# Kernel optimization log

Hardware: AMD Instinct MI355X
Metric: run time of the kernel (lower is better)

The kernel has to match this reference:

```python
import jax, jax.numpy as jnp
import numpy as np

E, T, H, I, K = 32, 2048, 1024, 512, 4


def setup_inputs() -> dict:
    key = jax.random.key(0)
    k1, k2, k3, k4, k5 = jax.random.split(key, 5)
    hidden_states = jax.random.normal(k1, (T, H), dtype=jnp.float32)
    top_k_index = jax.random.randint(k2, (T, K), 0, E)
    w = jax.random.uniform(k3, (T, K), dtype=jnp.float32)
    top_k_weights = w / jnp.sum(w, axis=-1, keepdims=True)  # router-like normalized weights
    gate_up_proj = jax.random.normal(k4, (E, 2 * I, H), dtype=jnp.float32) * 0.02
    down_proj = jax.random.normal(k5, (E, H, I), dtype=jnp.float32) * 0.02
    return {
        "hidden_states": hidden_states,
        "top_k_index": top_k_index,
        "top_k_weights": top_k_weights,
        "gate_up_proj": gate_up_proj,
        "down_proj": down_proj,
    }


def reference(hidden_states, top_k_index, top_k_weights, gate_up_proj, down_proj):
    # Faithful to the eager MoE dispatch loop: for each expert e, gather the
    # tokens routed to it, run gate/up/down SwiGLU, scale by routing weight,
    # and scatter-add into the output. Expressed as a scan over experts with a
    # per-token routing weight that is 0 for unrouted tokens (identical math:
    # index_add over (token, slot) pairs == sum_k where(idx==e, w, 0)).
    num_experts = gate_up_proj.shape[0]
    inter = down_proj.shape[2]

    def expert_step(acc, xs):
        gup_w, down_w, e = xs  # [2I, H], [H, I], scalar expert id
        # combined routing weight per token for this expert: [T]
        w_tok = jnp.sum(jnp.where(top_k_index == e, top_k_weights, 0.0), axis=1)
        gu = hidden_states @ gup_w.T              # [T, 2I]
        gate, up = gu[:, :inter], gu[:, inter:]
        h = jax.nn.silu(gate) * up                # [T, I]
        out = h @ down_w.T                        # [T, H]
        return acc + out * w_tok[:, None], None

    init = jnp.zeros_like(hidden_states)
    final_hidden_states, _ = jax.lax.scan(
        expert_step, init,
        (gate_up_proj, down_proj, jnp.arange(num_experts)),
    )
    return final_hidden_states
```

## Files before the change

### kernel.cpp

```cpp
#include <hip/hip_runtime.h>

#define NE 32
#define NT 2048
#define NH 1024
#define NI 512
#define NK 4
#define CAP 512

typedef __attribute__((ext_vector_type(8))) short short8;
typedef __attribute__((ext_vector_type(4))) float floatx4;

static __device__ __forceinline__ unsigned pk_bf16(float x, float y) {
#if __has_builtin(__builtin_amdgcn_cvt_pk_bf16_f32)
    typedef __attribute__((ext_vector_type(2))) __bf16 bf16x2;
    union { bf16x2 v; unsigned u; } c;
    c.v = __builtin_amdgcn_cvt_pk_bf16_f32(x, y);
    return c.u;
#else
    union { float f; unsigned u; } a, b;
    a.f = x; b.f = y;
    unsigned ua = (a.u + 0x7fffu + ((a.u >> 16) & 1u)) >> 16;
    unsigned ub = (b.u + 0x7fffu + ((b.u >> 16) & 1u)) >> 16;
    return (ua & 0xffffu) | (ub << 16);
#endif
}

static __device__ __forceinline__ short8 pack8(const float* p) {
    union { unsigned u[4]; short8 s; } c;
    c.u[0] = pk_bf16(p[0], p[1]);
    c.u[1] = pk_bf16(p[2], p[3]);
    c.u[2] = pk_bf16(p[4], p[5]);
    c.u[3] = pk_bf16(p[6], p[7]);
    return c.s;
}

static __device__ __forceinline__ unsigned short bf16_1(float x) {
    return (unsigned short)(pk_bf16(x, 0.f) & 0xffffu);
}

__global__ void route_kernel(const int* __restrict__ idx,
                             const float* __restrict__ w,
                             int* __restrict__ counts,
                             int* __restrict__ tok,
                             float* __restrict__ wgt) {
    int tid = blockIdx.x * blockDim.x + threadIdx.x;
    if (tid >= NT * NK) return;
    int e = idx[tid];
    int pos = atomicAdd(&counts[e], 1);
    if (pos < CAP) {
        tok[e * CAP + pos] = tid;
        wgt[e * CAP + pos] = w[tid];
    }
}

__global__ void cvt_hidden(const float* __restrict__ hidden,
                           unsigned short* __restrict__ hb16) {
    size_t i = (size_t)(blockIdx.x * 256 + threadIdx.x) * 8;
    float tmp[8];
    *(floatx4*)tmp       = *(const floatx4*)(hidden + i);
    *(floatx4*)(tmp + 4) = *(const floatx4*)(hidden + i + 4);
    *(short8*)(hb16 + i) = pack8(tmp);
}

__global__ __launch_bounds__(256) void gateup_mfma(
    const unsigned short* __restrict__ hb16,
    const float* __restrict__ gup,
    const int* __restrict__ counts,
    const int* __restrict__ tok,
    unsigned short* __restrict__ hbuf)
{
    int e = blockIdx.z;
    int cnt = counts[e];
    int m0 = blockIdx.y * 128;
    if (m0 >= cnt) return;
    int j0 = blockIdx.x * 64;

    __shared__ __align__(16) char smem[36864];
    __shared__ int tks[128];

    short (*As)[72] = (short(*)[72])smem;
    short (*Bs)[72] = (short(*)[72])(smem + 18432);
    float (*upb)[64][68] = (float(*)[64][68])smem;

    int tid = threadIdx.x;
    if (tid < 128) {
        int mi = m0 + tid;
        tks[tid] = tok[e * CAP + (mi < cnt ? mi : m0)];
    }
    __syncthreads();

    int srow = tid >> 1;
    int shalf = tid & 1;
    const unsigned short* ag = hb16 + (size_t)(tks[srow] >> 2) * NH + shalf * 32;
    const float* gup_e = gup + (size_t)e * (2 * NI) * NH;
    int gj = (srow < 64) ? (j0 + srow) : (NI + j0 + (srow - 64));
    const float* bg = gup_e + (size_t)gj * NH + shalf * 32;

    int wave = tid >> 6, lane = tid & 63;
    int wm = wave >> 1;
    int wv = wave & 1;
    int lcol = lane & 15;
    int quad = lane >> 4;
    int lk = quad * 8;

    floatx4 acc[4][4];
#pragma unroll
    for (int a = 0; a < 4; a++)
#pragma unroll
        for (int b = 0; b < 4; b++) acc[a][b] = (floatx4){0.f, 0.f, 0.f, 0.f};

    for (int h0 = 0; h0 < NH; h0 += 64) {
#pragma unroll
        for (int q = 0; q < 4; q++)
            *(short8*)&As[srow][shalf * 32 + q * 8] =
                *(const short8*)(ag + h0 + q * 8);
#pragma unroll
        for (int q = 0; q < 4; q++) {
            float tmp[8];
            *(floatx4*)tmp       = *(const floatx4*)(bg + h0 + q * 8);
            *(floatx4*)(tmp + 4) = *(const floatx4*)(bg + h0 + q * 8 + 4);
            *(short8*)&Bs[srow][shalf * 32 + q * 8] = pack8(tmp);
        }
        __syncthreads();
#pragma unroll
        for (int ks = 0; ks < 2; ks++) {
            short8 af[4], bfr[4];
#pragma unroll
            for (int mt = 0; mt < 4; mt++)
                af[mt] = *(const short8*)&As[wm * 64 + mt * 16 + lcol][ks * 32 + lk];
#pragma unroll
            for (int nt = 0; nt < 4; nt++)
                bfr[nt] = *(const short8*)&Bs[wv * 64 + nt * 16 + lcol][ks * 32 + lk];
#pragma unroll
            for (int mt = 0; mt < 4; mt++)
#pragma unroll
                for (int nt = 0; nt < 4; nt++)
                    acc[mt][nt] = __builtin_amdgcn_mfma_f32_16x16x32_bf16(
                        af[mt], bfr[nt], acc[mt][nt], 0, 0, 0);
        }
        __syncthreads();
    }

    if (wv == 1) {
#pragma unroll
        for (int mt = 0; mt < 4; mt++)
#pragma unroll
            for (int nt = 0; nt < 4; nt++)
#pragma unroll
                for (int i = 0; i < 4; i++)
                    upb[wm][mt * 16 + quad * 4 + i][nt * 16 + lcol] = acc[mt][nt][i];
    }
    __syncthreads();
    if (wv == 0) {
#pragma unroll
        for (int mt = 0; mt < 4; mt++) {
#pragma unroll
            for (int i = 0; i < 4; i++) {
                int lm = mt * 16 + quad * 4 + i;
                int m = wm * 64 + lm;
                if (m0 + m < cnt) {
                    unsigned short* hp = hbuf + (size_t)tks[m] * NI + j0;
#pragma unroll
                    for (int nt = 0; nt < 4; nt++) {
                        float g = acc[mt][nt][i];
                        float u = upb[wm][lm][nt * 16 + lcol];
                        float h = g / (1.f + __expf(-g)) * u;
                        hp[nt * 16 + lcol] = bf16_1(h);
                    }
                }
            }
        }
    }
}

__global__ __launch_bounds__(256) void down_mfma(
    const unsigned short* __restrict__ hbuf,
    const float* __restrict__ down,
    const int* __restrict__ counts,
    const int* __restrict__ tok,
    const float* __restrict__ wgt,
    float* __restrict__ out)
{
    int e = blockIdx.z;
    int cnt = counts[e];
    int m0 = blockIdx.y * 128;
    if (m0 >= cnt) return;
    int n0 = blockIdx.x * 128;

    __shared__ __align__(16) short As[128][72];
    __shared__ __align__(16) short Bs[128][72];
    __shared__ int tks[128];
    __shared__ float wls[128];

    int tid = threadIdx.x;
    if (tid < 128) {
        int mi = m0 + tid;
        int src = e * CAP + (mi < cnt ? mi : m0);
        tks[tid] = tok[src];
        wls[tid] = wgt[src];
    }
    __syncthreads();

    int srow = tid >> 1;
    int shalf = tid & 1;
    const unsigned short* ag = hbuf + (size_t)tks[srow] * NI + shalf * 32;
    const float* down_e = down + (size_t)e * NH * NI;
    const float* bg = down_e + (size_t)(n0 + srow) * NI + shalf * 32;

    int wave = tid >> 6, lane = tid & 63;
    int wm = wave >> 1, wn = wave & 1;
    int lcol = lane & 15;
    int quad = lane >> 4;
    int lk = quad * 8;

    floatx4 acc[4][4];
#pragma unroll
    for (int a = 0; a < 4; a++)
#pragma unroll
        for (int b = 0; b < 4; b++) acc[a][b] = (floatx4){0.f, 0.f, 0.f, 0.f};

    for (int i0 = 0; i0 < NI; i0 += 64) {
#pragma unroll
        for (int q = 0; q < 4; q++)
            *(short8*)&As[srow][shalf * 32 + q * 8] =
                *(const short8*)(ag + i0 + q * 8);
#pragma unroll
        for (int q = 0; q < 4; q++) {
            float tmp[8];
            *(floatx4*)tmp       = *(const floatx4*)(bg + i0 + q * 8);
            *(floatx4*)(tmp + 4) = *(const floatx4*)(bg + i0 + q * 8 + 4);
            *(short8*)&Bs[srow][shalf * 32 + q * 8] = pack8(tmp);
        }
        __syncthreads();
#pragma unroll
        for (int ks = 0; ks < 2; ks++) {
            short8 af[4], bfr[4];
#pragma unroll
            for (int mt = 0; mt < 4; mt++)
                af[mt] = *(const short8*)&As[wm * 64 + mt * 16 + lcol][ks * 32 + lk];
#pragma unroll
            for (int nt = 0; nt < 4; nt++)
                bfr[nt] = *(const short8*)&Bs[wn * 64 + nt * 16 + lcol][ks * 32 + lk];
#pragma unroll
            for (int mt = 0; mt < 4; mt++)
#pragma unroll
                for (int nt = 0; nt < 4; nt++)
                    acc[mt][nt] = __builtin_amdgcn_mfma_f32_16x16x32_bf16(
                        af[mt], bfr[nt], acc[mt][nt], 0, 0, 0);
        }
        __syncthreads();
    }

#pragma unroll
    for (int mt = 0; mt < 4; mt++)
#pragma unroll
        for (int i = 0; i < 4; i++) {
            int m = wm * 64 + mt * 16 + quad * 4 + i;
            if (m0 + m < cnt) {
                int t = tks[m] >> 2;
                float wl = wls[m];
                float* op = out + (size_t)t * NH + n0 + wn * 64;
#pragma unroll
                for (int nt = 0; nt < 4; nt++)
                    atomicAdd(op + nt * 16 + lcol, acc[mt][nt][i] * wl);
            }
        }
}

extern "C" void kernel_launch(void* const* d_in, const int* in_sizes, int n_in,
                              void* d_out, int out_size, void* d_ws, size_t ws_size,
                              hipStream_t stream) {
    const float* hidden = (const float*)d_in[0];
    const int*   tk_idx = (const int*)d_in[1];
    const float* tk_w   = (const float*)d_in[2];
    const float* gup    = (const float*)d_in[3];
    const float* down   = (const float*)d_in[4];
    float* out = (float*)d_out;

    char* ws = (char*)d_ws;
    int*            counts = (int*)ws;
    int*            tok    = (int*)(ws + 256);
    float*          wgt    = (float*)(ws + 256 + NE * CAP * 4);
    unsigned short* hb16   = (unsigned short*)(ws + 256 + 2 * NE * CAP * 4);
    unsigned short* hbuf   = (unsigned short*)(ws + 256 + 2 * NE * CAP * 4
                                               + (size_t)NT * NH * 2);

    hipMemsetAsync(counts, 0, 256, stream);
    hipMemsetAsync(out, 0, (size_t)NT * NH * sizeof(float), stream);

    route_kernel<<<(NT * NK + 255) / 256, 256, 0, stream>>>(tk_idx, tk_w, counts, tok, wgt);
    cvt_hidden<<<(NT * NH / 8) / 256, 256, 0, stream>>>(hidden, hb16);

    dim3 gridG(NI / 64, CAP / 128, NE);
    gateup_mfma<<<gridG, 256, 0, stream>>>(hb16, gup, counts, tok, hbuf);

    dim3 gridD(NH / 128, CAP / 128, NE);
    down_mfma<<<gridD, 256, 0, stream>>>(hbuf, down, counts, tok, wgt, out);
}
```

Before: 402.6 us.

## Register-prefetch next K tile and coalesce global loads in both expert GEMMs

Both grouped GEMM kernels now issue the global loads for the next K tile into registers right after the barrier, so they overlap with the MFMA work on the current tile, then write them to shared memory at the start of the next iteration. The thread-to-element mapping is also changed so adjacent threads read adjacent 16-byte chunks of a row, giving coalesced accesses instead of each thread streaming half a row. The cost is more live registers for the prefetch buffers, which may reduce occupancy.

```diff
diff --git a/kernel.cpp b/kernel.cpp
--- a/kernel.cpp
+++ b/kernel.cpp
@@ -89,12 +89,18 @@
     }
     __syncthreads();
 
-    int srow = tid >> 1;
-    int shalf = tid & 1;
-    const unsigned short* ag = hb16 + (size_t)(tks[srow] >> 2) * NH + shalf * 32;
+    int arow_base = tid >> 3;
+    int acol = (tid & 7) * 8;
+    const unsigned short* ap[4];
+#pragma unroll
+    for (int p = 0; p < 4; p++)
+        ap[p] = hb16 + (size_t)(tks[p * 32 + arow_base] >> 2) * NH + acol;
+
+    int brow_base = tid >> 4;
+    int bcol = (tid & 15) * 4;
     const float* gup_e = gup + (size_t)e * (2 * NI) * NH;
-    int gj = (srow < 64) ? (j0 + srow) : (NI + j0 + (srow - 64));
-    const float* bg = gup_e + (size_t)gj * NH + shalf * 32;
+    const float* bp0 = gup_e + (size_t)(j0 + brow_base) * NH + bcol;
+#define GUP_OFF(p) ((size_t)(p) * 16 * NH + ((p) >= 4 ? (size_t)(NI - 64) * NH : (size_t)0))
 
     int wave = tid >> 6, lane = tid & 63;
     int wm = wave >> 1;
@@ -109,19 +115,32 @@
 #pragma unroll
         for (int b = 0; b < 4; b++) acc[a][b] = (floatx4){0.f, 0.f, 0.f, 0.f};
 
+    short8 ra[4];
+    float4 rb[8];
+#pragma unroll
+    for (int p = 0; p < 4; p++) ra[p] = *(const short8*)(ap[p]);
+#pragma unroll
+    for (int p = 0; p < 8; p++) rb[p] = *(const float4*)(bp0 + GUP_OFF(p));
+
     for (int h0 = 0; h0 < NH; h0 += 64) {
 #pragma unroll
-        for (int q = 0; q < 4; q++)
-            *(short8*)&As[srow][shalf * 32 + q * 8] =
-                *(const short8*)(ag + h0 + q * 8);
-#pragma unroll
-        for (int q = 0; q < 4; q++) {
-            float tmp[8];
-            *(floatx4*)tmp       = *(const floatx4*)(bg + h0 + q * 8);
-            *(floatx4*)(tmp + 4) = *(const floatx4*)(bg + h0 + q * 8 + 4);
-            *(short8*)&Bs[srow][shalf * 32 + q * 8] = pack8(tmp);
+        for (int p = 0; p < 4; p++)
+            *(short8*)&As[p * 32 + arow_base][acol] = ra[p];
+#pragma unroll
+        for (int p = 0; p < 8; p++) {
+            uint2 u;
+            u.x = pk_bf16(rb[p].x, rb[p].y);
+            u.y = pk_bf16(rb[p].z, rb[p].w);
+            *(uint2*)&Bs[p * 16 + brow_base][bcol] = u;
         }
         __syncthreads();
+        int hn = h0 + 64;
+        if (hn < NH) {
+#pragma unroll
+            for (int p = 0; p < 4; p++) ra[p] = *(const short8*)(ap[p] + hn);
+#pragma unroll
+            for (int p = 0; p < 8; p++) rb[p] = *(const float4*)(bp0 + GUP_OFF(p) + hn);
+        }
 #pragma unroll
         for (int ks = 0; ks < 2; ks++) {
             short8 af[4], bfr[4];
@@ -201,11 +220,18 @@
     }
     __syncthreads();
 
-    int srow = tid >> 1;
-    int shalf = tid & 1;
-    const unsigned short* ag = hbuf + (size_t)tks[srow] * NI + shalf * 32;
+    int arow_base = tid >> 3;
+    int acol = (tid & 7) * 8;
+    const unsigned short* ap[4];
+#pragma unroll
+    for (int p = 0; p < 4; p++)
+        ap[p] = hbuf + (size_t)tks[p * 32 + arow_base] * NI + acol;
+
+    int brow_base = tid >> 4;
+    int bcol = (tid & 15) * 4;
     const float* down_e = down + (size_t)e * NH * NI;
-    const float* bg = down_e + (size_t)(n0 + srow) * NI + shalf * 32;
+    const float* bp0 = down_e + (size_t)(n0 + brow_base) * NI + bcol;
+#define DN_OFF(p) ((size_t)(p) * 16 * NI)
 
     int wave = tid >> 6, lane = tid & 63;
     int wm = wave >> 1, wn = wave & 1;
@@ -219,19 +245,32 @@
 #pragma unroll
         for (int b = 0; b < 4; b++) acc[a][b] = (floatx4){0.f, 0.f, 0.f, 0.f};
 
+    short8 ra[4];
+    float4 rb[8];
+#pragma unroll
+    for (int p = 0; p < 4; p++) ra[p] = *(const short8*)(ap[p]);
+#pragma unroll
+    for (int p = 0; p < 8; p++) rb[p] = *(const float4*)(bp0 + DN_OFF(p));
+
     for (int i0 = 0; i0 < NI; i0 += 64) {
 #pragma unroll
-        for (int q = 0; q < 4; q++)
-            *(short8*)&As[srow][shalf * 32 + q * 8] =
-                *(const short8*)(ag + i0 + q * 8);
-#pragma unroll
-        for (int q = 0; q < 4; q++) {
-            float tmp[8];
-            *(floatx4*)tmp       = *(const floatx4*)(bg + i0 + q * 8);
-            *(floatx4*)(tmp + 4) = *(const floatx4*)(bg + i0 + q * 8 + 4);
-            *(short8*)&Bs[srow][shalf * 32 + q * 8] = pack8(tmp);
+        for (int p = 0; p < 4; p++)
+            *(short8*)&As[p * 32 + arow_base][acol] = ra[p];
+#pragma unroll
+        for (int p = 0; p < 8; p++) {
+            uint2 u;
+            u.x = pk_bf16(rb[p].x, rb[p].y);
+            u.y = pk_bf16(rb[p].z, rb[p].w);
+            *(uint2*)&Bs[p * 16 + brow_base][bcol] = u;
         }
         __syncthreads();
+        int in = i0 + 64;
+        if (in < NI) {
+#pragma unroll
+            for (int p = 0; p < 4; p++) ra[p] = *(const short8*)(ap[p] + in);
+#pragma unroll
+            for (int p = 0; p < 8; p++) rb[p] = *(const float4*)(bp0 + DN_OFF(p) + in);
+        }
 #pragma unroll
         for (int ks = 0; ks < 2; ks++) {
             short8 af[4], bfr[4];
```

After: 339.6 us. -15.6%, faster.

## Double-buffer LDS with register prefetch and XOR swizzle in both MoE GEMMs

Applied to the files above, without the earlier changes.

Both expert GEMM kernels now use double-buffered LDS tiles. The next K-slice is prefetched into registers while MFMAs run on the current buffer, so each iteration needs one barrier instead of two. The padded LDS rows are replaced by an XOR-swizzled layout to avoid bank conflicts, and gate-up now assigns gate and up columns to the same wave so SwiGLU runs in registers without an LDS exchange. Occupancy hints (launch_bounds 256,2) and clamping of count to capacity are added, at the cost of more registers and more LDS per block.

```diff
diff --git a/kernel.cpp b/kernel.cpp
--- a/kernel.cpp
+++ b/kernel.cpp
@@ -62,7 +62,8 @@
     *(short8*)(hb16 + i) = pack8(tmp);
 }
 
-__global__ __launch_bounds__(256) void gateup_mfma(
+
+__global__ __launch_bounds__(256, 2) void gateup_mfma(
     const unsigned short* __restrict__ hb16,
     const float* __restrict__ gup,
     const int* __restrict__ counts,
@@ -70,38 +71,40 @@
     unsigned short* __restrict__ hbuf)
 {
     int e = blockIdx.z;
-    int cnt = counts[e];
+    int cnt = counts[e]; if (cnt > CAP) cnt = CAP;
     int m0 = blockIdx.y * 128;
     if (m0 >= cnt) return;
     int j0 = blockIdx.x * 64;
 
-    __shared__ __align__(16) char smem[36864];
-    __shared__ int tks[128];
-
-    short (*As)[72] = (short(*)[72])smem;
-    short (*Bs)[72] = (short(*)[72])(smem + 18432);
-    float (*upb)[64][68] = (float(*)[64][68])smem;
+    __shared__ __align__(16) short As[2][128][64];
+    __shared__ __align__(16) short Bs[2][128][64];
 
     int tid = threadIdx.x;
-    if (tid < 128) {
-        int mi = m0 + tid;
-        tks[tid] = tok[e * CAP + (mi < cnt ? mi : m0)];
-    }
-    __syncthreads();
-
-    int srow = tid >> 1;
-    int shalf = tid & 1;
-    const unsigned short* ag = hb16 + (size_t)(tks[srow] >> 2) * NH + shalf * 32;
+    int sr = tid >> 3;
+    int sg = tid & 7;
+
+    const unsigned short* aptr[4];
+    short* awr[4];
+    const float* bptr[4];
+    short* bwr[4];
     const float* gup_e = gup + (size_t)e * (2 * NI) * NH;
-    int gj = (srow < 64) ? (j0 + srow) : (NI + j0 + (srow - 64));
-    const float* bg = gup_e + (size_t)gj * NH + shalf * 32;
+#pragma unroll
+    for (int p = 0; p < 4; p++) {
+        int r = p * 32 + sr;
+        int mi = m0 + r;
+        int tk = tok[e * CAP + (mi < cnt ? mi : m0)];
+        aptr[p] = hb16 + (size_t)(tk >> 2) * NH + sg * 8;
+        awr[p]  = &As[0][r][(sg ^ (r & 7)) * 8];
+        int gj = (r < 64) ? (j0 + r) : (NI + j0 + (r - 64));
+        bptr[p] = gup_e + (size_t)gj * NH + sg * 8;
+        bwr[p]  = &Bs[0][r][(sg ^ (r & 7)) * 8];
+    }
 
     int wave = tid >> 6, lane = tid & 63;
     int wm = wave >> 1;
-    int wv = wave & 1;
+    int wj = wave & 1;
     int lcol = lane & 15;
     int quad = lane >> 4;
-    int lk = quad * 8;
 
     floatx4 acc[4][4];
 #pragma unroll
@@ -109,28 +112,51 @@
 #pragma unroll
         for (int b = 0; b < 4; b++) acc[a][b] = (floatx4){0.f, 0.f, 0.f, 0.f};
 
-    for (int h0 = 0; h0 < NH; h0 += 64) {
-#pragma unroll
-        for (int q = 0; q < 4; q++)
-            *(short8*)&As[srow][shalf * 32 + q * 8] =
-                *(const short8*)(ag + h0 + q * 8);
-#pragma unroll
-        for (int q = 0; q < 4; q++) {
-            float tmp[8];
-            *(floatx4*)tmp       = *(const floatx4*)(bg + h0 + q * 8);
-            *(floatx4*)(tmp + 4) = *(const floatx4*)(bg + h0 + q * 8 + 4);
-            *(short8*)&Bs[srow][shalf * 32 + q * 8] = pack8(tmp);
-        }
-        __syncthreads();
+    short8 ra[4];
+    float4 rb[8];
+#pragma unroll
+    for (int p = 0; p < 4; p++) {
+        ra[p] = *(const short8*)(aptr[p]);
+        rb[2 * p]     = *(const float4*)(bptr[p]);
+        rb[2 * p + 1] = *(const float4*)(bptr[p] + 4);
+    }
+#pragma unroll
+    for (int p = 0; p < 4; p++) {
+        *(short8*)(awr[p]) = ra[p];
+        union { unsigned u[4]; short8 s; } c;
+        c.u[0] = pk_bf16(rb[2 * p].x, rb[2 * p].y);
+        c.u[1] = pk_bf16(rb[2 * p].z, rb[2 * p].w);
+        c.u[2] = pk_bf16(rb[2 * p + 1].x, rb[2 * p + 1].y);
+        c.u[3] = pk_bf16(rb[2 * p + 1].z, rb[2 * p + 1].w);
+        *(short8*)(bwr[p]) = c.s;
+    }
+#pragma unroll
+    for (int p = 0; p < 4; p++) {
+        ra[p] = *(const short8*)(aptr[p] + 64);
+        rb[2 * p]     = *(const float4*)(bptr[p] + 64);
+        rb[2 * p + 1] = *(const float4*)(bptr[p] + 68);
+    }
+    __syncthreads();
+
+    const int NIT = NH / 64;
+    for (int it = 0; it < NIT; ++it) {
+        int cur = it & 1;
+        int co = cur * 8192;
 #pragma unroll
         for (int ks = 0; ks < 2; ks++) {
             short8 af[4], bfr[4];
-#pragma unroll
-            for (int mt = 0; mt < 4; mt++)
-                af[mt] = *(const short8*)&As[wm * 64 + mt * 16 + lcol][ks * 32 + lk];
-#pragma unroll
-            for (int nt = 0; nt < 4; nt++)
-                bfr[nt] = *(const short8*)&Bs[wv * 64 + nt * 16 + lcol][ks * 32 + lk];
+            int q = ks * 4 + quad;
+#pragma unroll
+            for (int mt = 0; mt < 4; mt++) {
+                int R = wm * 64 + mt * 16 + lcol;
+                af[mt] = *(const short8*)&As[cur][R][(q ^ (R & 7)) * 8];
+            }
+#pragma unroll
+            for (int nt = 0; nt < 4; nt++) {
+                int R = (nt < 2) ? (wj * 32 + nt * 16 + lcol)
+                                 : (64 + wj * 32 + (nt - 2) * 16 + lcol);
+                bfr[nt] = *(const short8*)&Bs[cur][R][(q ^ (R & 7)) * 8];
+            }
 #pragma unroll
             for (int mt = 0; mt < 4; mt++)
 #pragma unroll
@@ -138,42 +164,52 @@
                     acc[mt][nt] = __builtin_amdgcn_mfma_f32_16x16x32_bf16(
                         af[mt], bfr[nt], acc[mt][nt], 0, 0, 0);
         }
-        __syncthreads();
-    }
-
-    if (wv == 1) {
-#pragma unroll
-        for (int mt = 0; mt < 4; mt++)
-#pragma unroll
-            for (int nt = 0; nt < 4; nt++)
-#pragma unroll
-                for (int i = 0; i < 4; i++)
-                    upb[wm][mt * 16 + quad * 4 + i][nt * 16 + lcol] = acc[mt][nt][i];
-    }
-    __syncthreads();
-    if (wv == 0) {
-#pragma unroll
-        for (int mt = 0; mt < 4; mt++) {
-#pragma unroll
-            for (int i = 0; i < 4; i++) {
-                int lm = mt * 16 + quad * 4 + i;
-                int m = wm * 64 + lm;
-                if (m0 + m < cnt) {
-                    unsigned short* hp = hbuf + (size_t)tks[m] * NI + j0;
-#pragma unroll
-                    for (int nt = 0; nt < 4; nt++) {
-                        float g = acc[mt][nt][i];
-                        float u = upb[wm][lm][nt * 16 + lcol];
-                        float h = g / (1.f + __expf(-g)) * u;
-                        hp[nt * 16 + lcol] = bf16_1(h);
-                    }
+        if (it + 1 < NIT) {
+            int no = (co ^ 8192);
+#pragma unroll
+            for (int p = 0; p < 4; p++) {
+                *(short8*)(awr[p] + no) = ra[p];
+                union { unsigned u[4]; short8 s; } c;
+                c.u[0] = pk_bf16(rb[2 * p].x, rb[2 * p].y);
+                c.u[1] = pk_bf16(rb[2 * p].z, rb[2 * p].w);
+                c.u[2] = pk_bf16(rb[2 * p + 1].x, rb[2 * p + 1].y);
+                c.u[3] = pk_bf16(rb[2 * p + 1].z, rb[2 * p + 1].w);
+                *(short8*)(bwr[p] + no) = c.s;
+            }
+            if (it + 2 < NIT) {
+                int h2 = (it + 2) * 64;
+#pragma unroll
+                for (int p = 0; p < 4; p++) {
+                    ra[p] = *(const short8*)(aptr[p] + h2);
+                    rb[2 * p]     = *(const float4*)(bptr[p] + h2);
+                    rb[2 * p + 1] = *(const float4*)(bptr[p] + h2 + 4);
                 }
             }
-        }
-    }
-}
-
-__global__ __launch_bounds__(256) void down_mfma(
+            __syncthreads();
+        }
+    }
+
+#pragma unroll
+    for (int mt = 0; mt < 4; mt++) {
+#pragma unroll
+        for (int i = 0; i < 4; i++) {
+            int m = wm * 64 + mt * 16 + quad * 4 + i;
+            if (m0 + m < cnt) {
+                int tk = tok[e * CAP + m0 + m];
+                unsigned short* hp = hbuf + (size_t)tk * NI + j0 + wj * 32 + lcol;
+#pragma unroll
+                for (int nt = 0; nt < 2; nt++) {
+                    float g = acc[mt][nt][i];
+                    float u = acc[mt][nt + 2][i];
+                    float h = g / (1.f + __expf(-g)) * u;
+                    hp[nt * 16] = bf16_1(h);
+                }
+            }
+        }
+    }
+}
+
+__global__ __launch_bounds__(256, 2) void down_mfma(
     const unsigned short* __restrict__ hbuf,
     const float* __restrict__ down,
     const int* __restrict__ counts,
@@ -182,36 +218,38 @@
     float* __restrict__ out)
 {
     int e = blockIdx.z;
-    int cnt = counts[e];
+    int cnt = counts[e]; if (cnt > CAP) cnt = CAP;
     int m0 = blockIdx.y * 128;
     if (m0 >= cnt) return;
     int n0 = blockIdx.x * 128;
 
-    __shared__ __align__(16) short As[128][72];
-    __shared__ __align__(16) short Bs[128][72];
-    __shared__ int tks[128];
-    __shared__ float wls[128];
+    __shared__ __align__(16) short As[2][128][64];
+    __shared__ __align__(16) short Bs[2][128][64];
 
     int tid = threadIdx.x;
-    if (tid < 128) {
-        int mi = m0 + tid;
-        int src = e * CAP + (mi < cnt ? mi : m0);
-        tks[tid] = tok[src];
-        wls[tid] = wgt[src];
-    }
-    __syncthreads();
-
-    int srow = tid >> 1;
-    int shalf = tid & 1;
-    const unsigned short* ag = hbuf + (size_t)tks[srow] * NI + shalf * 32;
+    int sr = tid >> 3;
+    int sg = tid & 7;
+
+    const unsigned short* aptr[4];
+    short* awr[4];
+    const float* bptr[4];
+    short* bwr[4];
     const float* down_e = down + (size_t)e * NH * NI;
-    const float* bg = down_e + (size_t)(n0 + srow) * NI + shalf * 32;
+#pragma unroll
+    for (int p = 0; p < 4; p++) {
+        int r = p * 32 + sr;
+        int mi = m0 + r;
+        int tk = tok[e * CAP + (mi < cnt ? mi : m0)];
+        aptr[p] = hbuf + (size_t)tk * NI + sg * 8;
+        awr[p]  = &As[0][r][(sg ^ (r & 7)) * 8];
+        bptr[p] = down_e + (size_t)(n0 + r) * NI + sg * 8;
+        bwr[p]  = &Bs[0][r][(sg ^ (r & 7)) * 8];
+    }
 
     int wave = tid >> 6, lane = tid & 63;
     int wm = wave >> 1, wn = wave & 1;
     int lcol = lane & 15;
     int quad = lane >> 4;
-    int lk = quad * 8;
 
     floatx4 acc[4][4];
 #pragma unroll
@@ -219,28 +257,49 @@
 #pragma unroll
         for (int b = 0; b < 4; b++) acc[a][b] = (floatx4){0.f, 0.f, 0.f, 0.f};
 
-    for (int i0 = 0; i0 < NI; i0 += 64) {
-#pragma unroll
-        for (int q = 0; q < 4; q++)
-            *(short8*)&As[srow][shalf * 32 + q * 8] =
-                *(const short8*)(ag + i0 + q * 8);
-#pragma unroll
-        for (int q = 0; q < 4; q++) {
-            float tmp[8];
-            *(floatx4*)tmp       = *(const floatx4*)(bg + i0 + q * 8);
-            *(floatx4*)(tmp + 4) = *(const floatx4*)(bg + i0 + q * 8 + 4);
-            *(short8*)&Bs[srow][shalf * 32 + q * 8] = pack8(tmp);
-        }
-        __syncthreads();
+    short8 ra[4];
+    float4 rb[8];
+#pragma unroll
+    for (int p = 0; p < 4; p++) {
+        ra[p] = *(const short8*)(aptr[p]);
+        rb[2 * p]     = *(const float4*)(bptr[p]);
+        rb[2 * p + 1] = *(const float4*)(bptr[p] + 4);
+    }
+#pragma unroll
+    for (int p = 0; p < 4; p++) {
+        *(short8*)(awr[p]) = ra[p];
+        union { unsigned u[4]; short8 s; } c;
+        c.u[0] = pk_bf16(rb[2 * p].x, rb[2 * p].y);
+        c.u[1] = pk_bf16(rb[2 * p].z, rb[2 * p].w);
+        c.u[2] = pk_bf16(rb[2 * p + 1].x, rb[2 * p + 1].y);
+        c.u[3] = pk_bf16(rb[2 * p + 1].z, rb[2 * p + 1].w);
+        *(short8*)(bwr[p]) = c.s;
+    }
+#pragma unroll
+    for (int p = 0; p < 4; p++) {
+        ra[p] = *(const short8*)(aptr[p] + 64);
+        rb[2 * p]     = *(const float4*)(bptr[p] + 64);
+        rb[2 * p + 1] = *(const float4*)(bptr[p] + 68);
+    }
+    __syncthreads();
+
+    const int NIT = NI / 64;
+    for (int it = 0; it < NIT; ++it) {
+        int cur = it & 1;
 #pragma unroll
         for (int ks = 0; ks < 2; ks++) {
             short8 af[4], bfr[4];
-#pragma unroll
-            for (int mt = 0; mt < 4; mt++)
-                af[mt] = *(const short8*)&As[wm * 64 + mt * 16 + lcol][ks * 32 + lk];
-#pragma unroll
-            for (int nt = 0; nt < 4; nt++)
-                bfr[nt] = *(const short8*)&Bs[wn * 64 + nt * 16 + lcol][ks * 32 + lk];
+            int q = ks * 4 + quad;
+#pragma unroll
+            for (int mt = 0; mt < 4; mt++) {
+                int R = wm * 64 + mt * 16 + lcol;
+                af[mt] = *(const short8*)&As[cur][R][(q ^ (R & 7)) * 8];
+            }
+#pragma unroll
+            for (int nt = 0; nt < 4; nt++) {
+                int R = wn * 64 + nt * 16 + lcol;
+                bfr[nt] = *(const short8*)&Bs[cur][R][(q ^ (R & 7)) * 8];
+            }
 #pragma unroll
             for (int mt = 0; mt < 4; mt++)
 #pragma unroll
@@ -248,7 +307,29 @@
                     acc[mt][nt] = __builtin_amdgcn_mfma_f32_16x16x32_bf16(
                         af[mt], bfr[nt], acc[mt][nt], 0, 0, 0);
         }
-        __syncthreads();
+        if (it + 1 < NIT) {
+            int no = ((cur ^ 1)) * 8192;
+#pragma unroll
+            for (int p = 0; p < 4; p++) {
+                *(short8*)(awr[p] + no) = ra[p];
+                union { unsigned u[4]; short8 s; } c;
+                c.u[0] = pk_bf16(rb[2 * p].x, rb[2 * p].y);
+                c.u[1] = pk_bf16(rb[2 * p].z, rb[2 * p].w);
+                c.u[2] = pk_bf16(rb[2 * p + 1].x, rb[2 * p + 1].y);
+                c.u[3] = pk_bf16(rb[2 * p + 1].z, rb[2 * p + 1].w);
+                *(short8*)(bwr[p] + no) = c.s;
+            }
+            if (it + 2 < NIT) {
+                int i2 = (it + 2) * 64;
+#pragma unroll
+                for (int p = 0; p < 4; p++) {
+                    ra[p] = *(const short8*)(aptr[p] + i2);
+                    rb[2 * p]     = *(const float4*)(bptr[p] + i2);
+                    rb[2 * p + 1] = *(const float4*)(bptr[p] + i2 + 4);
+                }
+            }
+            __syncthreads();
+        }
     }
 
 #pragma unroll
@@ -257,12 +338,12 @@
         for (int i = 0; i < 4; i++) {
             int m = wm * 64 + mt * 16 + quad * 4 + i;
             if (m0 + m < cnt) {
-                int t = tks[m] >> 2;
-                float wl = wls[m];
-                float* op = out + (size_t)t * NH + n0 + wn * 64;
+                int tk = tok[e * CAP + m0 + m];
+                float wl = wgt[e * CAP + m0 + m];
+                float* op = out + (size_t)(tk >> 2) * NH + n0 + wn * 64 + lcol;
 #pragma unroll
                 for (int nt = 0; nt < 4; nt++)
-                    atomicAdd(op + nt * 16 + lcol, acc[mt][nt][i] * wl);
+                    atomicAdd(op + nt * 16, acc[mt][nt][i] * wl);
             }
         }
 }
```

Result: faster. 346.0 us (-14.1%).
